# Kernel optimization log

Hardware: AMD Instinct MI355X
Metric: run time of the kernel (lower is better)

The kernel has to match this reference:

```python
import jax
import jax.numpy as jnp
from jax import lax
import numpy as np

N_NODES = 1_000_000
DEGREE = 31            # neighbors per agent -> group_size = DEGREE + 1
GROUP = DEGREE + 1
THRESHOLD = 16         # CRD threshold M = group_size / 2
COST = 0.25            # CRD cooperation cost c


def setup_inputs() -> dict:
    key = jax.random.key(0)
    k1, k2 = jax.random.split(key)
    gains = jax.random.normal(k1, (N_NODES,), dtype=jnp.float32)
    neighbors = jax.random.randint(k2, (N_NODES, DEGREE), 0, N_NODES, dtype=jnp.int64)
    return {"gains": gains, "neighbors": neighbors}


def reference(gains, neighbors):
    # sigmoid cooperation prob per agent, then neighbor gather -> [N, GROUP]
    p = jax.nn.sigmoid(gains)                       # [N]
    group_p = jnp.concatenate([p[:, None], p[neighbors]], axis=1)  # [N, GROUP]

    # Poisson-Binomial PMF via DP convolution over group members.
    # dp[n, k] = P(k cooperators among members processed so far)
    n = group_p.shape[0]
    dp0 = jnp.zeros((n, GROUP + 1), dtype=group_p.dtype).at[:, 0].set(1.0)

    def step(dp, pj):  # pj: [N] coop prob of one group member
        pj = pj[:, None]
        shifted = jnp.pad(dp[:, :-1], ((0, 0), (1, 0)))  # dp shifted by one success
        return dp * (1.0 - pj) + shifted * pj, None

    dp, _ = lax.scan(step, dp0, group_p.T)          # scan over GROUP members

    prob_above = dp[:, THRESHOLD:].sum(axis=1)      # P(count >= THRESHOLD), [N]
    acum_loss = jnp.sum(prob_above - COST * p)
    return -acum_loss
```

## Files before the change

### kernel.cpp

```cpp
#include <hip/hip_runtime.h>

constexpr int DEG = 31;
constexpr int NEV = 32;
constexpr int TH  = 16;
constexpr int BLK = 256;
constexpr int TBL = 1 << 20;

constexpr int CH    = 1 << 16;
constexpr int NPASS = TBL / CH;
constexpr int BLK2  = 1024;
constexpr int NPB   = 2048;

typedef int  vint4  __attribute__((ext_vector_type(4)));

__global__ void zero_out_kernel(float* out) {
    if (threadIdx.x == 0) out[0] = 0.0f;
}

__device__ __forceinline__ float fast_sigmoid(float x) {
    return 1.0f / (1.0f + __expf(-x));
}

__global__ __launch_bounds__(256)
void build_table_kernel(const float* __restrict__ gains,
                        unsigned* __restrict__ tbl4,
                        float* __restrict__ out, int n) {
    const int t = blockIdx.x * 256 + threadIdx.x;
    if (t == 0) out[0] = 0.0f;
    if (t < TBL / 4) {
        unsigned w = 0;
        #pragma unroll
        for (int k = 0; k < 4; ++k) {
            const int i = 4 * t + k;
            const float p = (i < n) ? fast_sigmoid(gains[i]) : 0.0f;
            const unsigned b = __float2uint_rn(p * 255.0f);
            w |= (b & 0xFFu) << (8 * k);
        }
        tbl4[t] = w;
    }
}

__device__ __forceinline__ float node_dp(float g, const unsigned w[8]) {
    const float p0 = fast_sigmoid(g);
    float dp[TH];
    dp[0] = 1.0f;
    #pragma unroll
    for (int k = 1; k < TH; ++k) dp[k] = 0.0f;
    float over = 0.0f;
    #pragma unroll
    for (int j = 0; j < NEV; ++j) {
        float pj;
        if (j == 0) {
            pj = p0;
        } else {
            const unsigned b = (w[(j - 1) >> 2] >> (((j - 1) & 3) * 8)) & 0xFFu;
            pj = (float)b * (1.0f / 255.0f);
        }
        if (j >= TH - 1) over = fmaf(dp[TH - 1], pj, over);
        const int kmax = (j + 1 < TH - 1) ? (j + 1) : (TH - 1);
        #pragma unroll
        for (int k = kmax; k >= 1; --k)
            dp[k] = fmaf(pj, dp[k - 1] - dp[k], dp[k]);
        dp[0] = fmaf(-pj, dp[0], dp[0]);
    }
    return fmaf(0.25f, p0, -over);
}

__global__ __launch_bounds__(BLK2, 4)
void pgl2_kernel(const float* __restrict__ gains,
                 const int*   __restrict__ nbr,
                 const unsigned char* __restrict__ tbl,
                 float*       __restrict__ out, int n) {
    __shared__ __align__(16) unsigned char smem[CH];

    const int tid        = threadIdx.x;
    const int blockStart = blockIdx.x * NPB;
    const int rows_total = min(NPB, n - blockStart);

    unsigned idxA[DEG], idxB[DEG];
    #pragma unroll
    for (int j = 0; j < DEG; ++j) { idxA[j] = 0u; idxB[j] = 0u; }

    #pragma unroll
    for (int r = 0; r < 4; ++r) {
        const int rowsR = max(0, min(512, rows_total - r * 512));
        const int elems = rowsR * DEG;
        const int base  = (blockStart + r * 512) * DEG;
        const vint4* nb4 = (const vint4*)(nbr + base);
        vint4* s4 = (vint4*)smem;
        const int nvec = elems >> 2;
        for (int v = tid; v < nvec; v += BLK2)
            s4[v] = __builtin_nontemporal_load(nb4 + v);
        for (int e = (nvec << 2) + tid; e < elems; e += BLK2)
            ((int*)smem)[e] = __builtin_nontemporal_load(nbr + base + e);
        __syncthreads();
        const int half = r & 1;
        const int s    = tid - half * 512;
        if (s >= 0 && s < rowsR) {
            const int* row = (const int*)smem + s * DEG;
            if ((r >> 1) == 0) {
                #pragma unroll
                for (int j = 0; j < DEG; ++j) idxA[j] = (unsigned)row[j];
            } else {
                #pragma unroll
                for (int j = 0; j < DEG; ++j) idxB[j] = (unsigned)row[j];
            }
        }
        __syncthreads();
    }

    unsigned wA[8], wB[8];
    #pragma unroll
    for (int q = 0; q < 8; ++q) { wA[q] = 0u; wB[q] = 0u; }

    #pragma unroll 1
    for (int c = 0; c < NPASS; ++c) {
        {
            const vint4* t4 = (const vint4*)(tbl + (size_t)c * CH);
            vint4* s4 = (vint4*)smem;
            #pragma unroll
            for (int q = 0; q < CH / 16 / BLK2; ++q)
                s4[q * BLK2 + tid] = t4[q * BLK2 + tid];
        }
        __syncthreads();

        const unsigned base = (unsigned)c * (unsigned)CH;
        #pragma unroll
        for (int j = 0; j < DEG; ++j) {
            const unsigned rA = idxA[j] - base;
            if (rA < (unsigned)CH)
                wA[j >> 2] |= (unsigned)smem[rA] << ((j & 3) * 8);
            const unsigned rB = idxB[j] - base;
            if (rB < (unsigned)CH)
                wB[j >> 2] |= (unsigned)smem[rB] << ((j & 3) * 8);
        }
        __syncthreads();
    }

    float local = 0.0f;
    const int iA = blockStart + tid;
    const int iB = blockStart + 1024 + tid;
    if (iA < n) local += node_dp(__builtin_nontemporal_load(gains + iA), wA);
    if (iB < n) local += node_dp(__builtin_nontemporal_load(gains + iB), wB);

    #pragma unroll
    for (int o = 32; o > 0; o >>= 1) local += __shfl_down(local, o, 64);
    float* s_red = (float*)smem;
    if ((tid & 63) == 0) s_red[tid >> 6] = local;
    __syncthreads();
    if (tid == 0) {
        float s = 0.0f;
        #pragma unroll
        for (int w = 0; w < BLK2 / 64; ++w) s += s_red[w];
        atomicAdd(out, s);
    }
}

__global__ __launch_bounds__(BLK)
void pgl_direct_kernel(const float* __restrict__ gains,
                       const int*   __restrict__ nbr,
                       float*       __restrict__ out, int n) {
    __shared__ int s_idx[BLK * DEG];
    __shared__ float s_red[BLK / 64];
    const int tid = threadIdx.x;
    const int blockStart = blockIdx.x * BLK;
    const int rows  = min(BLK, n - blockStart);
    const int elems = rows * DEG;
    const int base  = blockStart * DEG;
    const int4* nb4 = (const int4*)(nbr + base);
    int4* s4 = (int4*)s_idx;
    const int nvec = elems >> 2;
    for (int v = tid; v < nvec; v += BLK) s4[v] = nb4[v];
    for (int e = (nvec << 2) + tid; e < elems; e += BLK) s_idx[e] = nbr[base + e];
    __syncthreads();
    float local = 0.0f;
    const int i = blockStart + tid;
    if (i < n) {
        const int* row = s_idx + tid * DEG;
        float dp[TH];
        dp[0] = 1.0f;
        #pragma unroll
        for (int k = 1; k < TH; ++k) dp[k] = 0.0f;
        float over = 0.0f;
        const float p0 = fast_sigmoid(gains[i]);
        #pragma unroll
        for (int j = 0; j < NEV; ++j) {
            const float pj = (j == 0) ? p0 : fast_sigmoid(gains[row[j - 1]]);
            if (j >= TH - 1) over = fmaf(dp[TH - 1], pj, over);
            const int kmax = (j + 1 < TH - 1) ? (j + 1) : (TH - 1);
            #pragma unroll
            for (int k = kmax; k >= 1; --k)
                dp[k] = fmaf(pj, dp[k - 1] - dp[k], dp[k]);
            dp[0] = fmaf(-pj, dp[0], dp[0]);
        }
        local = fmaf(0.25f, p0, -over);
    }
    #pragma unroll
    for (int o = 32; o > 0; o >>= 1) local += __shfl_down(local, o, 64);
    if ((tid & 63) == 0) s_red[tid >> 6] = local;
    __syncthreads();
    if (tid == 0) {
        float s = 0.0f;
        #pragma unroll
        for (int w = 0; w < BLK / 64; ++w) s += s_red[w];
        atomicAdd(out, s);
    }
}

extern "C" void kernel_launch(void* const* d_in, const int* in_sizes, int n_in,
                              void* d_out, int out_size, void* d_ws, size_t ws_size,
                              hipStream_t stream) {
    const float* gains = (const float*)d_in[0];
    const int*   nbr   = (const int*)d_in[1];
    float*       out   = (float*)d_out;
    const int n = in_sizes[0];

    if (ws_size >= (size_t)TBL && n <= TBL) {
        unsigned char* tbl = (unsigned char*)d_ws;
        build_table_kernel<<<(TBL / 4 + 255) / 256, 256, 0, stream>>>(
            gains, (unsigned*)tbl, out, n);
        const int grid2 = (n + NPB - 1) / NPB;
        pgl2_kernel<<<grid2, BLK2, 0, stream>>>(gains, nbr, tbl, out, n);
    } else {
        zero_out_kernel<<<1, 64, 0, stream>>>(out);
        const int grid = (n + BLK - 1) / BLK;
        pgl_direct_kernel<<<grid, BLK, 0, stream>>>(gains, nbr, out, n);
    }
}
```

Measured before the change: 305.9 us.

## Split block into LDS-scan and direct-gather warp roles

Restructures the lookup kernel so half the threads stream the byte table through shared memory in 64KB chunks while the other half issue direct global byte loads for their neighbors. Each role handles 512 rows per half-iteration, processed in two halves, which reduces idx register footprint and allows higher occupancy (launch bounds raised to 8 waves per EU). The aim is to overlap gather latency with the LDS scan and halve the per-thread scan work. The risks are that direct gathers hit random cache lines, that the table is now streamed twice per block, and that the raw barriers with hand-placed waitcnts could be fragile.

```diff
diff --git a/kernel.cpp b/kernel.cpp
--- a/kernel.cpp
+++ b/kernel.cpp
@@ -8,7 +8,7 @@
 
 constexpr int CH    = 1 << 16;
 constexpr int NPASS = TBL / CH;
-constexpr int BLK2  = 1024;
+constexpr int BLKF  = 1024;
 constexpr int NPB   = 2048;
 
 typedef int  vint4  __attribute__((ext_vector_type(4)));
@@ -19,6 +19,12 @@
 
 __device__ __forceinline__ float fast_sigmoid(float x) {
     return 1.0f / (1.0f + __expf(-x));
+}
+
+__device__ __forceinline__ void barrier_raw() {
+    asm volatile("" ::: "memory");
+    __builtin_amdgcn_s_barrier();
+    asm volatile("" ::: "memory");
 }
 
 __global__ __launch_bounds__(256)
@@ -66,92 +72,117 @@
     return fmaf(0.25f, p0, -over);
 }
 
-__global__ __launch_bounds__(BLK2, 4)
-void pgl2_kernel(const float* __restrict__ gains,
-                 const int*   __restrict__ nbr,
-                 const unsigned char* __restrict__ tbl,
-                 float*       __restrict__ out, int n) {
+__global__ __launch_bounds__(BLKF, 8)
+void pgl_fused_kernel(const float* __restrict__ gains,
+                      const int*   __restrict__ nbr,
+                      const unsigned char* __restrict__ tbl,
+                      float*       __restrict__ out, int n) {
     __shared__ __align__(16) unsigned char smem[CH];
 
-    const int tid        = threadIdx.x;
-    const int blockStart = blockIdx.x * NPB;
-    const int rows_total = min(NPB, n - blockStart);
-
-    unsigned idxA[DEG], idxB[DEG];
-    #pragma unroll
-    for (int j = 0; j < DEG; ++j) { idxA[j] = 0u; idxB[j] = 0u; }
-
-    #pragma unroll
-    for (int r = 0; r < 4; ++r) {
-        const int rowsR = max(0, min(512, rows_total - r * 512));
-        const int elems = rowsR * DEG;
-        const int base  = (blockStart + r * 512) * DEG;
-        const vint4* nb4 = (const vint4*)(nbr + base);
-        vint4* s4 = (vint4*)smem;
-        const int nvec = elems >> 2;
-        for (int v = tid; v < nvec; v += BLK2)
-            s4[v] = __builtin_nontemporal_load(nb4 + v);
-        for (int e = (nvec << 2) + tid; e < elems; e += BLK2)
-            ((int*)smem)[e] = __builtin_nontemporal_load(nbr + base + e);
-        __syncthreads();
-        const int half = r & 1;
-        const int s    = tid - half * 512;
-        if (s >= 0 && s < rowsR) {
-            const int* row = (const int*)smem + s * DEG;
-            if ((r >> 1) == 0) {
+    const int  tid      = threadIdx.x;
+    const bool scanRole = (tid < 512);
+    const int  blockStart = blockIdx.x * NPB;
+
+    float local = 0.0f;
+
+    #pragma unroll 1
+    for (int half = 0; half < 2; ++half) {
+        unsigned idx[DEG];
+        #pragma unroll 1
+        for (int rnd = 0; rnd < 2; ++rnd) {
+            const int rowBase = blockStart + rnd * 1024 + half * 512;
+            const int rowsR   = min(512, max(0, n - rowBase));
+            const int elems   = rowsR * DEG;
+            __syncthreads();
+            {
+                const vint4* nb4 = (const vint4*)(nbr + (size_t)rowBase * DEG);
+                vint4* s4 = (vint4*)smem;
+                const int nvec = elems >> 2;
+                for (int v = tid; v < nvec; v += BLKF)
+                    s4[v] = __builtin_nontemporal_load(nb4 + v);
+                for (int e = (nvec << 2) + tid; e < elems; e += BLKF)
+                    ((int*)smem)[e] = __builtin_nontemporal_load(nbr + (size_t)rowBase * DEG + e);
+            }
+            __syncthreads();
+            const bool myRound = (rnd == 0) ? scanRole : !scanRole;
+            if (myRound) {
+                const int s = scanRole ? tid : (tid - 512);
+                if (s < rowsR) {
+                    const int* row = (const int*)smem + s * DEG;
+                    #pragma unroll
+                    for (int j = 0; j < DEG; ++j) idx[j] = (unsigned)row[j];
+                } else {
+                    #pragma unroll
+                    for (int j = 0; j < DEG; ++j) idx[j] = 0u;
+                }
+            }
+        }
+
+        unsigned w[8];
+        #pragma unroll
+        for (int q = 0; q < 8; ++q) w[q] = 0u;
+
+        unsigned gb[DEG];
+        if (!scanRole) {
+            #pragma unroll
+            for (int j = 0; j < DEG; ++j) {
+                const unsigned char* ap = tbl + idx[j];
+                unsigned v;
+                asm volatile("global_load_ubyte %0, %1, off" : "=v"(v) : "v"(ap));
+                gb[j] = v;
+            }
+        }
+
+        #pragma unroll 1
+        for (int c = 0; c < NPASS; ++c) {
+            barrier_raw();
+            if (scanRole) {
+                const vint4* src = (const vint4*)(tbl + (size_t)c * CH);
+                vint4* dst = (vint4*)smem;
+                vint4 t0 = src[0 * 512 + tid], t1 = src[1 * 512 + tid],
+                      t2 = src[2 * 512 + tid], t3 = src[3 * 512 + tid];
+                dst[0 * 512 + tid] = t0; dst[1 * 512 + tid] = t1;
+                dst[2 * 512 + tid] = t2; dst[3 * 512 + tid] = t3;
+                t0 = src[4 * 512 + tid]; t1 = src[5 * 512 + tid];
+                t2 = src[6 * 512 + tid]; t3 = src[7 * 512 + tid];
+                dst[4 * 512 + tid] = t0; dst[5 * 512 + tid] = t1;
+                dst[6 * 512 + tid] = t2; dst[7 * 512 + tid] = t3;
+                asm volatile("s_waitcnt lgkmcnt(0)" ::: "memory");
+            }
+            barrier_raw();
+            if (scanRole) {
+                const unsigned cbase = (unsigned)c * (unsigned)CH;
                 #pragma unroll
-                for (int j = 0; j < DEG; ++j) idxA[j] = (unsigned)row[j];
-            } else {
-                #pragma unroll
-                for (int j = 0; j < DEG; ++j) idxB[j] = (unsigned)row[j];
-            }
-        }
-        __syncthreads();
-    }
-
-    unsigned wA[8], wB[8];
-    #pragma unroll
-    for (int q = 0; q < 8; ++q) { wA[q] = 0u; wB[q] = 0u; }
-
-    #pragma unroll 1
-    for (int c = 0; c < NPASS; ++c) {
-        {
-            const vint4* t4 = (const vint4*)(tbl + (size_t)c * CH);
-            vint4* s4 = (vint4*)smem;
+                for (int j = 0; j < DEG; ++j) {
+                    const unsigned r = idx[j] - cbase;
+                    if (r < (unsigned)CH)
+                        w[j >> 2] |= (unsigned)smem[r] << ((j & 3) * 8);
+                }
+            }
+        }
+
+        if (!scanRole) {
+            asm volatile("s_waitcnt vmcnt(0)" ::: "memory");
+            __builtin_amdgcn_sched_barrier(0);
             #pragma unroll
-            for (int q = 0; q < CH / 16 / BLK2; ++q)
-                s4[q * BLK2 + tid] = t4[q * BLK2 + tid];
-        }
-        __syncthreads();
-
-        const unsigned base = (unsigned)c * (unsigned)CH;
-        #pragma unroll
-        for (int j = 0; j < DEG; ++j) {
-            const unsigned rA = idxA[j] - base;
-            if (rA < (unsigned)CH)
-                wA[j >> 2] |= (unsigned)smem[rA] << ((j & 3) * 8);
-            const unsigned rB = idxB[j] - base;
-            if (rB < (unsigned)CH)
-                wB[j >> 2] |= (unsigned)smem[rB] << ((j & 3) * 8);
-        }
-        __syncthreads();
-    }
-
-    float local = 0.0f;
-    const int iA = blockStart + tid;
-    const int iB = blockStart + 1024 + tid;
-    if (iA < n) local += node_dp(__builtin_nontemporal_load(gains + iA), wA);
-    if (iB < n) local += node_dp(__builtin_nontemporal_load(gains + iB), wB);
+            for (int j = 0; j < DEG; ++j)
+                w[j >> 2] |= (gb[j] & 0xFFu) << ((j & 3) * 8);
+        }
+
+        const int node = blockStart + half * 512 + tid + (scanRole ? 0 : 512);
+        if (node < n)
+            local += node_dp(__builtin_nontemporal_load(gains + node), w);
+    }
 
     #pragma unroll
     for (int o = 32; o > 0; o >>= 1) local += __shfl_down(local, o, 64);
-    float* s_red = (float*)smem;
-    if ((tid & 63) == 0) s_red[tid >> 6] = local;
+    __syncthreads();
+    if ((tid & 63) == 0) ((float*)smem)[tid >> 6] = local;
     __syncthreads();
     if (tid == 0) {
         float s = 0.0f;
         #pragma unroll
-        for (int w = 0; w < BLK2 / 64; ++w) s += s_red[w];
+        for (int wv = 0; wv < BLKF / 64; ++wv) s += ((float*)smem)[wv];
         atomicAdd(out, s);
     }
 }
@@ -219,8 +250,8 @@
         unsigned char* tbl = (unsigned char*)d_ws;
         build_table_kernel<<<(TBL / 4 + 255) / 256, 256, 0, stream>>>(
             gains, (unsigned*)tbl, out, n);
-        const int grid2 = (n + NPB - 1) / NPB;
-        pgl2_kernel<<<grid2, BLK2, 0, stream>>>(gains, nbr, tbl, out, n);
+        const int gridF = (n + NPB - 1) / NPB;
+        pgl_fused_kernel<<<gridF, BLKF, 0, stream>>>(gains, nbr, tbl, out, n);
     } else {
         zero_out_kernel<<<1, 64, 0, stream>>>(out);
         const int grid = (n + BLK - 1) / BLK;
```

Measured after the change: 363.7 us. 18.9% more time.

## Stage 128KB table chunks via direct global-to-LDS loads with batched lookups

Applied to the files above, without the earlier changes.

Doubles the shared-memory chunk of the quantized probability table to 128KB, which halves the number of passes. Table chunks are copied straight into LDS with global_load_lds instead of going through registers. The neighbor-index staging now takes two 1024-row passes, and the per-chunk lookups are batched eight at a time with clamped addresses to expose more LDS load parallelism. The larger LDS footprint limits occupancy to one block per CU, so load latency may be hidden less well.

```diff
diff --git a/kernel.cpp b/kernel.cpp
--- a/kernel.cpp
+++ b/kernel.cpp
@@ -6,10 +6,10 @@
 constexpr int BLK = 256;
 constexpr int TBL = 1 << 20;
 
-constexpr int CH    = 1 << 16;
+constexpr int CH    = 1 << 17;
 constexpr int NPASS = TBL / CH;
-constexpr int BLK2  = 1024;
-constexpr int NPB   = 2048;
+constexpr int BLK4  = 1024;
+constexpr int NPB4  = 2048;
 
 typedef int  vint4  __attribute__((ext_vector_type(4)));
 
@@ -66,39 +66,42 @@
     return fmaf(0.25f, p0, -over);
 }
 
-__global__ __launch_bounds__(BLK2, 4)
-void pgl2_kernel(const float* __restrict__ gains,
+__global__ __launch_bounds__(BLK4, 4)
+void pgl4_kernel(const float* __restrict__ gains,
                  const int*   __restrict__ nbr,
                  const unsigned char* __restrict__ tbl,
                  float*       __restrict__ out, int n) {
     __shared__ __align__(16) unsigned char smem[CH];
 
     const int tid        = threadIdx.x;
-    const int blockStart = blockIdx.x * NPB;
-    const int rows_total = min(NPB, n - blockStart);
+    const int wid        = tid >> 6;
+    const int lane       = tid & 63;
+    const int blockStart = blockIdx.x * NPB4;
 
     unsigned idxA[DEG], idxB[DEG];
     #pragma unroll
     for (int j = 0; j < DEG; ++j) { idxA[j] = 0u; idxB[j] = 0u; }
 
-    #pragma unroll
-    for (int r = 0; r < 4; ++r) {
-        const int rowsR = max(0, min(512, rows_total - r * 512));
-        const int elems = rowsR * DEG;
-        const int base  = (blockStart + r * 512) * DEG;
-        const vint4* nb4 = (const vint4*)(nbr + base);
-        vint4* s4 = (vint4*)smem;
-        const int nvec = elems >> 2;
-        for (int v = tid; v < nvec; v += BLK2)
-            s4[v] = __builtin_nontemporal_load(nb4 + v);
-        for (int e = (nvec << 2) + tid; e < elems; e += BLK2)
-            ((int*)smem)[e] = __builtin_nontemporal_load(nbr + base + e);
-        __syncthreads();
-        const int half = r & 1;
-        const int s    = tid - half * 512;
-        if (s >= 0 && s < rowsR) {
-            const int* row = (const int*)smem + s * DEG;
-            if ((r >> 1) == 0) {
+    #pragma unroll 1
+    for (int r = 0; r < 2; ++r) {
+        const int rowBase = blockStart + r * 1024;
+        const int rows    = min(1024, max(0, n - rowBase));
+        const int elems   = rows * DEG;
+        __syncthreads();
+        {
+            const size_t base = (size_t)rowBase * DEG;
+            const vint4* nb4  = (const vint4*)(nbr + base);
+            vint4* s4 = (vint4*)smem;
+            const int nvec = elems >> 2;
+            for (int v = tid; v < nvec; v += BLK4)
+                s4[v] = __builtin_nontemporal_load(nb4 + v);
+            for (int e = (nvec << 2) + tid; e < elems; e += BLK4)
+                ((int*)smem)[e] = __builtin_nontemporal_load(nbr + base + e);
+        }
+        __syncthreads();
+        if (tid < rows) {
+            const int* row = (const int*)smem + tid * DEG;
+            if (r == 0) {
                 #pragma unroll
                 for (int j = 0; j < DEG; ++j) idxA[j] = (unsigned)row[j];
             } else {
@@ -106,7 +109,6 @@
                 for (int j = 0; j < DEG; ++j) idxB[j] = (unsigned)row[j];
             }
         }
-        __syncthreads();
     }
 
     unsigned wA[8], wB[8];
@@ -115,26 +117,45 @@
 
     #pragma unroll 1
     for (int c = 0; c < NPASS; ++c) {
+        __syncthreads();
+
         {
-            const vint4* t4 = (const vint4*)(tbl + (size_t)c * CH);
-            vint4* s4 = (vint4*)smem;
-            #pragma unroll
-            for (int q = 0; q < CH / 16 / BLK2; ++q)
-                s4[q * BLK2 + tid] = t4[q * BLK2 + tid];
-        }
-        __syncthreads();
-
-        const unsigned base = (unsigned)c * (unsigned)CH;
-        #pragma unroll
-        for (int j = 0; j < DEG; ++j) {
-            const unsigned rA = idxA[j] - base;
-            if (rA < (unsigned)CH)
-                wA[j >> 2] |= (unsigned)smem[rA] << ((j & 3) * 8);
-            const unsigned rB = idxB[j] - base;
-            if (rB < (unsigned)CH)
-                wB[j >> 2] |= (unsigned)smem[rB] << ((j & 3) * 8);
-        }
-        __syncthreads();
+            const size_t gbase = (size_t)c * (size_t)CH;
+            #pragma unroll
+            for (int q = 0; q < 8; ++q) {
+                const int off = q * 16384 + wid * 1024;
+                const unsigned char* src = tbl + gbase + (size_t)off + (size_t)lane * 16;
+                __builtin_amdgcn_global_load_lds(
+                    (const __attribute__((address_space(1))) void*)src,
+                    (__attribute__((address_space(3))) void*)(smem + off),
+                    16, 0, 0);
+            }
+        }
+        __syncthreads();
+
+        const unsigned cbase = (unsigned)c * (unsigned)CH;
+        #pragma unroll
+        for (int jb = 0; jb < DEG; jb += 8) {
+            const int m = (jb + 8 <= DEG) ? 8 : (DEG - jb);
+            unsigned rA[8], bA[8], rB[8], bB[8];
+            #pragma unroll
+            for (int u = 0; u < m; ++u) {
+                rA[u] = idxA[jb + u] - cbase;
+                const unsigned aA = (rA[u] < (unsigned)CH) ? rA[u] : (unsigned)(CH - 1);
+                bA[u] = (unsigned)smem[aA];
+                rB[u] = idxB[jb + u] - cbase;
+                const unsigned aB = (rB[u] < (unsigned)CH) ? rB[u] : (unsigned)(CH - 1);
+                bB[u] = (unsigned)smem[aB];
+            }
+            #pragma unroll
+            for (int u = 0; u < m; ++u) {
+                const int j = jb + u;
+                wA[j >> 2] |= (rA[u] < (unsigned)CH)
+                                  ? ((bA[u] & 0xFFu) << ((j & 3) * 8)) : 0u;
+                wB[j >> 2] |= (rB[u] < (unsigned)CH)
+                                  ? ((bB[u] & 0xFFu) << ((j & 3) * 8)) : 0u;
+            }
+        }
     }
 
     float local = 0.0f;
@@ -145,13 +166,13 @@
 
     #pragma unroll
     for (int o = 32; o > 0; o >>= 1) local += __shfl_down(local, o, 64);
-    float* s_red = (float*)smem;
-    if ((tid & 63) == 0) s_red[tid >> 6] = local;
+    __syncthreads();
+    if ((tid & 63) == 0) ((float*)smem)[tid >> 6] = local;
     __syncthreads();
     if (tid == 0) {
         float s = 0.0f;
         #pragma unroll
-        for (int w = 0; w < BLK2 / 64; ++w) s += s_red[w];
+        for (int wv = 0; wv < BLK4 / 64; ++wv) s += ((float*)smem)[wv];
         atomicAdd(out, s);
     }
 }
@@ -219,8 +240,8 @@
         unsigned char* tbl = (unsigned char*)d_ws;
         build_table_kernel<<<(TBL / 4 + 255) / 256, 256, 0, stream>>>(
             gains, (unsigned*)tbl, out, n);
-        const int grid2 = (n + NPB - 1) / NPB;
-        pgl2_kernel<<<grid2, BLK2, 0, stream>>>(gains, nbr, tbl, out, n);
+        const int grid4 = (n + NPB4 - 1) / NPB4;
+        pgl4_kernel<<<grid4, BLK4, 0, stream>>>(gains, nbr, tbl, out, n);
     } else {
         zero_out_kernel<<<1, 64, 0, stream>>>(out);
         const int grid = (n + BLK - 1) / BLK;
```

Result: faster. 298.8 us (-2.3%).
